# Optimization experiments

Measured on AMD Instinct MI355X. Metric: run time of the kernel, lower is better.

The kernel has to match this reference:

```python
import jax, jax.numpy as jnp
import numpy as np

N = 8192
G = 12972
EPS = 1e-5


def setup_inputs() -> dict:
    key = jax.random.key(0)
    ks = jax.random.split(key, 8)
    # solutions: one-hot letters per position -> (N, 26, 5)
    sol_letters = jax.random.randint(ks[0], (N, 5), 0, 26)
    sols = jax.nn.one_hot(sol_letters, 26, dtype=jnp.float32).transpose(0, 2, 1)
    # guess vocabulary: one-hot words -> (G, 130) with (26,5) layout flattened
    g_letters = jax.random.randint(ks[1], (G, 5), 0, 26)
    guesses_mat = jax.nn.one_hot(g_letters, 26, dtype=jnp.float32).transpose(0, 2, 1).reshape(G, 130)
    s0 = 1.0 / np.sqrt(292.0)
    sh = 1.0 / np.sqrt(1000.0)
    W0 = jax.random.normal(ks[2], (292, 1000), jnp.float32) * s0
    b0 = jnp.zeros((1000,), jnp.float32)
    gammas = jnp.ones((4, 1000), jnp.float32)
    betas = jnp.zeros((4, 1000), jnp.float32)
    Wh = jax.random.normal(ks[3], (3, 1000, 1000), jnp.float32) * sh
    bh = jnp.zeros((3, 1000), jnp.float32)
    Wout = jax.random.normal(ks[4], (1000, 130), jnp.float32) * sh
    bout = jnp.zeros((130,), jnp.float32)
    return {"sols": sols, "guesses_mat": guesses_mat, "W0": W0, "b0": b0,
            "gammas": gammas, "betas": betas, "Wh": Wh, "bh": bh,
            "Wout": Wout, "bout": bout}


def _mlp(X, W0, b0, gammas, betas, Wh, bh, Wout, bout):
    h = X @ W0 + b0
    for i in range(4):
        mu = h.mean(axis=0)
        var = ((h - mu) ** 2).mean(axis=0)  # biased variance, as torch BN training
        h = gammas[i] * (h - mu) * jax.lax.rsqrt(var + EPS) + betas[i]
        h = jnp.where(h >= 0, h, 0.2 * h)
        if i < 3:
            h = h @ Wh[i] + bh[i]
        else:
            h = h @ Wout + bout
    return h


def reference(sols, guesses_mat, W0, b0, gammas, betas, Wh, bh, Wout, bout):
    n = sols.shape[0]
    hints = jnp.zeros((n, 286), jnp.float32)
    scores = 7.0 * jnp.ones((n,), jnp.float32)
    total_loss = jnp.float32(0.0)
    first_guess = None
    solved = jnp.zeros((n,), bool)
    sols_letters = jnp.clip(sols.sum(axis=2), 0.0, 1.0)[:, :, None]  # (n,26,1)
    for turn in range(6):
        turn_vec = jnp.zeros((n, 6), jnp.float32).at[:, turn].set(1.0)
        X = jnp.concatenate((hints, turn_vec), axis=1)  # (n, 292)
        y = _mlp(X, W0, b0, gammas, betas, Wh, bh, Wout, bout).reshape(n, 26, 5)
        logp = jax.nn.log_softmax(y, axis=1)
        loss = -(sols * logp).sum(axis=1).mean()
        if turn >= 1:
            total_loss = total_loss + loss
        y_soft = jax.nn.softmax(y, axis=1).reshape(n, 130)
        # nearest-guess retrieval: argmax over vocab of dot products, then gather
        sim = y_soft @ guesses_mat.T  # (n, G)
        idx = jnp.argmax(sim, axis=1)
        nudges = jax.lax.stop_gradient(guesses_mat[idx] - y_soft)
        guesses = (y_soft + nudges).reshape(n, 26, 5)
        if turn == 0:
            first_guess = guesses[0]
        greens = guesses * sols
        yellows = (1.0 - greens) * (guesses * sols_letters)
        blacks = (guesses * (1.0 - greens) * (1.0 - yellows)).sum(axis=2)  # (n,26)
        solved = greens.reshape(n, -1).sum(axis=1) == 5.0
        new_hints = jnp.concatenate((greens.reshape(n, 130), yellows.reshape(n, 130), blacks), axis=1)
        hints = hints + new_hints
        scores = jnp.where((scores > turn + 1) & solved, jnp.float32(turn + 1), scores)
    return total_loss, scores.sum(), solved.sum(), first_guess
```

## Files before the change

kernel.cpp:

```cpp
#include <hip/hip_runtime.h>

#define NROWS 8192
#define NG    12972
#define H     1000
#define NP    1024
#define KX    288
#define OCP   256
#define OC    130
#define EPSBN 1e-5f
#define MBLK  (NROWS / 128)

typedef __attribute__((ext_vector_type(8))) _Float16 f16x8;
typedef __attribute__((ext_vector_type(8))) unsigned short u16x8;
typedef __attribute__((ext_vector_type(4))) float f32x4;

__device__ __forceinline__ float lrelu(float x) { return x >= 0.f ? x : 0.2f * x; }

__global__ void transpose_f16(const float* __restrict__ src, int R, int C, int srcStride,
                              _Float16* __restrict__ dst, int Rp, int Cp) {
    __shared__ float tile[32][33];
    int k0 = blockIdx.x * 32;
    int n0 = blockIdx.y * 32;
    int tx = threadIdx.x, ty = threadIdx.y;
#pragma unroll
    for (int i = 0; i < 32; i += 8) {
        int k = k0 + ty + i, n = n0 + tx;
        tile[ty + i][tx] = (k < R && n < C) ? src[(size_t)k * srcStride + n] : 0.f;
    }
    __syncthreads();
#pragma unroll
    for (int i = 0; i < 32; i += 8) {
        int n = n0 + ty + i, k = k0 + tx;
        if (n < Cp && k < Rp) dst[(size_t)n * Rp + k] = (_Float16)tile[tx][ty + i];
    }
}

__global__ void prep_bias(const float* __restrict__ W0, const float* __restrict__ b0,
                          const float* __restrict__ bh, const float* __restrict__ bout,
                          float* __restrict__ b0p, float* __restrict__ w0t,
                          float* __restrict__ bhp, float* __restrict__ boutp) {
    int i = blockIdx.x * 256 + threadIdx.x;
    if (i < 1024) { b0p[i] = (i < H) ? b0[i] : 0.f; return; }
    i -= 1024;
    if (i < 6 * 1024) {
        int t = i >> 10, n = i & 1023;
        w0t[i] = (n < H) ? W0[(size_t)(286 + t) * H + n] : 0.f;
        return;
    }
    i -= 6 * 1024;
    if (i < 3 * 1024) {
        int l = i >> 10, n = i & 1023;
        bhp[i] = (n < H) ? bh[l * H + n] : 0.f;
        return;
    }
    i -= 3 * 1024;
    if (i < OCP) { boutp[i] = (i < OC) ? bout[i] : 0.f; }
}

__global__ void prep_guess_letters(const float* __restrict__ gm, unsigned char* __restrict__ gl,
                                   uint2* __restrict__ glp) {
    int g = blockIdx.x * blockDim.x + threadIdx.x;
    if (g >= NG) return;
    unsigned off[5];
    for (int p = 0; p < 5; ++p) {
        int letter = 0;
        for (int c = 0; c < 26; ++c)
            if (gm[(size_t)g * 130 + c * 5 + p] > 0.5f) { letter = c; break; }
        gl[g * 8 + p] = (unsigned char)letter;
        off[p] = (unsigned)(letter * 5 + p);
    }
    gl[g * 8 + 5] = gl[g * 8 + 6] = gl[g * 8 + 7] = 0;
    glp[g] = make_uint2(off[0] | (off[1] << 8) | (off[2] << 16) | (off[3] << 24), off[4]);
}

__global__ void prep_sol_letters(const float* __restrict__ sols, unsigned char* __restrict__ sl,
                                 unsigned int* __restrict__ msk) {
    int r = blockIdx.x * blockDim.x + threadIdx.x;
    if (r >= NROWS) return;
    unsigned int m = 0;
    for (int p = 0; p < 5; ++p) {
        int letter = 0;
        for (int c = 0; c < 26; ++c)
            if (sols[(size_t)r * 130 + c * 5 + p] > 0.5f) { letter = c; break; }
        sl[r * 8 + p] = (unsigned char)letter;
        m |= 1u << letter;
    }
    sl[r * 8 + 5] = sl[r * 8 + 6] = sl[r * 8 + 7] = 0;
    msk[r] = m;
}

__global__ void init_state(unsigned short* __restrict__ hX, float* __restrict__ scores,
                           int* __restrict__ solvedf, float* __restrict__ lossacc) {
    int i = blockIdx.x * blockDim.x + threadIdx.x;
    if (i < NROWS * KX) hX[i] = 0;
    if (i < NROWS) { scores[i] = 7.f; solvedf[i] = 0; }
    if (i == 0) lossacc[0] = 0.f;
}

template <int BK, bool HALF_C>
__global__ __launch_bounds__(256, 2) void gemm_f16(
    const _Float16* __restrict__ A, int lda,
    const _Float16* __restrict__ B, int ldb,
    void* __restrict__ Cv, int ldc,
    const float* __restrict__ bias1, const float* __restrict__ bias2, int kiter,
    float* __restrict__ pS, float* __restrict__ pS2) {
    constexpr int NCH = BK / 8;
    constexpr int ABYTES = 256 * BK;
    constexpr int KSUB = BK / 32;
    constexpr int AW = 16 * BK;
    __shared__ char smem[512 * BK];
    const int tid = threadIdx.x;
    const int lane = tid & 63;
    const int rowBase = blockIdx.x * 128;
    const int colBase = blockIdx.y * 128;
    const int wm = (tid >> 6) & 1;
    const int wn = tid >> 7;

    const _Float16* gsrc[NCH];
    int ldsuni[NCH];
#pragma unroll
    for (int i = 0; i < NCH; ++i) {
        int w = i * 256 + tid;
        const _Float16* plane;
        int off;
        if (w < AW) {
            int r = w & 127, kb = w >> 7;
            plane = A;
            off = (rowBase + r) * lda + kb * 8;
        } else {
            int v = w - AW;
            int col = v & 127, kb = v >> 7;
            plane = B;
            off = (colBase + col) * ldb + kb * 8;
        }
        gsrc[i] = plane + off;
        ldsuni[i] = (i * 256 + (tid & ~63)) * 16;
    }

    f32x4 acc[4][4];
    const f32x4 z = {0.f, 0.f, 0.f, 0.f};
#pragma unroll
    for (int m = 0; m < 4; ++m)
#pragma unroll
        for (int n = 0; n < 4; ++n) acc[m][n] = z;

    const int aro = (lane >> 4) * 2048 + (wm * 64 + (lane & 15)) * 16;
    const int bco = ABYTES + (lane >> 4) * 2048 + (wn * 64 + (lane & 15)) * 16;

    for (int t = 0; t < kiter; ++t) {
#pragma unroll
        for (int i = 0; i < NCH; ++i)
            __builtin_amdgcn_global_load_lds(
                (const __attribute__((address_space(1))) void*)(gsrc[i] + (size_t)t * BK),
                (__attribute__((address_space(3))) void*)(smem + ldsuni[i]), 16, 0, 0);
        __syncthreads();

        f16x8 a_f[KSUB][4], b_f[KSUB][4];
#pragma unroll
        for (int ks = 0; ks < KSUB; ++ks) {
#pragma unroll
            for (int m = 0; m < 4; ++m) a_f[ks][m] = *(const f16x8*)(smem + ks * 8192 + aro + m * 256);
#pragma unroll
            for (int n = 0; n < 4; ++n) b_f[ks][n] = *(const f16x8*)(smem + ks * 8192 + bco + n * 256);
        }
#pragma unroll
        for (int ks = 0; ks < KSUB; ++ks)
#pragma unroll
            for (int m = 0; m < 4; ++m)
#pragma unroll
                for (int n = 0; n < 4; ++n)
                    acc[m][n] = __builtin_amdgcn_mfma_f32_16x16x32_f16(a_f[ks][m], b_f[ks][n],
                                                                       acc[m][n], 0, 0, 0);
        __syncthreads();
    }

    float* sS  = (float*)smem;
    float* sS2 = (float*)smem + 256;
    const int lane16 = lane & 15, lanehi = lane >> 4;
#pragma unroll
    for (int n = 0; n < 4; ++n) {
        int col = colBase + wn * 64 + n * 16 + lane16;
        float bv = bias1[col] + (bias2 ? bias2[col] : 0.f);
        float s = 0.f, s2 = 0.f;
#pragma unroll
        for (int m = 0; m < 4; ++m) {
            int row0 = rowBase + wm * 64 + m * 16 + lanehi * 4;
#pragma unroll
            for (int r = 0; r < 4; ++r) {
                float cv = acc[m][n][r] + bv;
                if constexpr (HALF_C)
                    ((_Float16*)Cv)[(size_t)(row0 + r) * ldc + col] = (_Float16)cv;
                else
                    ((float*)Cv)[(size_t)(row0 + r) * ldc + col] = cv;
                s += cv; s2 += cv * cv;
            }
        }
        if (pS) {
            s += __shfl_xor(s, 16);  s += __shfl_xor(s, 32);
            s2 += __shfl_xor(s2, 16); s2 += __shfl_xor(s2, 32);
            if (lanehi == 0) {
                int lcol = wn * 64 + n * 16 + lane16;
                sS[wm * 128 + lcol] = s;
                sS2[wm * 128 + lcol] = s2;
            }
        }
    }
    if (pS) {
        __syncthreads();
        if (tid < 128) {
            int col = colBase + tid;
            pS[(size_t)blockIdx.x * NP + col] = sS[tid] + sS[128 + tid];
            pS2[(size_t)blockIdx.x * NP + col] = sS2[tid] + sS2[128 + tid];
        }
    }
}

__global__ __launch_bounds__(256) void bn_apply_f(
    const _Float16* __restrict__ hraw, const float* __restrict__ pS, const float* __restrict__ pS2,
    const float* __restrict__ gamma, const float* __restrict__ beta,
    _Float16* __restrict__ oh) {
    __shared__ float la[128], lb[128];
    const int tid = threadIdx.x;
    const int rowBase = blockIdx.x * 128;
    const int colBase = blockIdx.y * 128;
    if (tid < 128) {
        int col = colBase + tid;
        float s = 0.f;
        for (int j = 0; j < MBLK; ++j) s += pS[(size_t)j * NP + col];
        la[tid] = s;
    } else {
        int col = colBase + tid - 128;
        float s2 = 0.f;
        for (int j = 0; j < MBLK; ++j) s2 += pS2[(size_t)j * NP + col];
        lb[tid - 128] = s2;
    }
    __syncthreads();
    if (tid < 128) {
        int col = colBase + tid;
        float a = 0.f, b = 0.f;
        if (col < H) {
            float mean = la[tid] * (1.f / NROWS);
            float var = lb[tid] * (1.f / NROWS) - mean * mean;
            float inv = rsqrtf(var + EPSBN);
            a = gamma[col] * inv;
            b = beta[col] - mean * a;
        }
        la[tid] = a;
        lb[tid] = b;
    }
    __syncthreads();
    const int c8 = (tid & 15) * 8;
    float ar[8], br[8];
#pragma unroll
    for (int j = 0; j < 8; ++j) { ar[j] = la[c8 + j]; br[j] = lb[c8 + j]; }
#pragma unroll
    for (int i = 0; i < 8; ++i) {
        int row = i * 16 + (tid >> 4);
        const u16x8 v = *(const u16x8*)(hraw + (size_t)(rowBase + row) * NP + colBase + c8);
        u16x8 o;
#pragma unroll
        for (int j = 0; j < 8; ++j) {
            float x = (float)__builtin_bit_cast(_Float16, (unsigned short)v[j]);
            o[j] = __builtin_bit_cast(unsigned short, (_Float16)lrelu(ar[j] * x + br[j]));
        }
        *(u16x8*)((unsigned short*)oh + (size_t)(rowBase + row) * NP + colBase + c8) = o;
    }
}

__global__ __launch_bounds__(256) void post_turn(
    const float* __restrict__ ybuf, const uint2* __restrict__ glp,
    const unsigned char* __restrict__ gl, const unsigned char* __restrict__ sl,
    const unsigned int* __restrict__ msk, _Float16* __restrict__ hX,
    float* __restrict__ scores, int* __restrict__ solvedf, float* __restrict__ lossacc,
    const float* __restrict__ gm, float* __restrict__ dout, int turn) {
    const int r0 = blockIdx.x * 8;
    __shared__ float pk[8][132];
    __shared__ float lcon[40];
    __shared__ float wb[4][8];
    __shared__ int wi[4][8];
    __shared__ int fidx[8];
    const int tid = threadIdx.x;

    if (tid < 40) {
        int row = tid / 5, p = tid - row * 5;
        const float* yr = ybuf + (size_t)(r0 + row) * OCP + p;
        float m = -1e30f;
#pragma unroll
        for (int c = 0; c < 26; ++c) m = fmaxf(m, yr[c * 5]);
        float e[26];
        float s = 0.f;
#pragma unroll
        for (int c = 0; c < 26; ++c) { e[c] = expf(yr[c * 5] - m); s += e[c]; }
        float inv = 1.f / s;
#pragma unroll
        for (int c = 0; c < 26; ++c) pk[row][c * 5 + p] = e[c] * inv;
        lcon[tid] = logf(s) + m - yr[sl[(size_t)(r0 + row) * 8 + p] * 5];
    }
    __syncthreads();

    float bb[8];
    int ii[8];
#pragma unroll
    for (int r = 0; r < 8; ++r) { bb[r] = -1e30f; ii[r] = 1 << 30; }
    for (int g = tid; g < NG; g += 256) {
        uint2 w = glp[g];
        int o0 = w.x & 255, o1 = (w.x >> 8) & 255, o2 = (w.x >> 16) & 255,
            o3 = w.x >> 24, o4 = w.y & 255;
#pragma unroll
        for (int r = 0; r < 8; ++r) {
            float v = pk[r][o0] + pk[r][o1]; v += pk[r][o2]; v += pk[r][o3]; v += pk[r][o4];
            if (v > bb[r]) { bb[r] = v; ii[r] = g; }
        }
    }
#pragma unroll
    for (int off = 1; off < 64; off <<= 1) {
#pragma unroll
        for (int r = 0; r < 8; ++r) {
            float o = __shfl_xor(bb[r], off);
            int oi = __shfl_xor(ii[r], off);
            if (o > bb[r] || (o == bb[r] && oi < ii[r])) { bb[r] = o; ii[r] = oi; }
        }
    }
    const int wid = tid >> 6, lane = tid & 63;
    if (lane == 0) {
#pragma unroll
        for (int r = 0; r < 8; ++r) { wb[wid][r] = bb[r]; wi[wid][r] = ii[r]; }
    }
    __syncthreads();

    if (tid < 8) {
        float b = wb[0][tid]; int x = wi[0][tid];
#pragma unroll
        for (int wv = 1; wv < 4; ++wv)
            if (wb[wv][tid] > b || (wb[wv][tid] == b && wi[wv][tid] < x)) { b = wb[wv][tid]; x = wi[wv][tid]; }
        fidx[tid] = x;
        int r = r0 + tid;
        const unsigned char* q = gl + x * 8;
        const unsigned char* so = sl + (size_t)r * 8;
        unsigned int mk = msk[r];
        _Float16* hrow = hX + (size_t)r * KX;
        int allg = 1;
#pragma unroll
        for (int p = 0; p < 5; ++p) {
            int g = q[p];
            int off;
            if (g == so[p]) {
                off = g * 5 + p;
            } else {
                allg = 0;
                off = ((mk >> g) & 1u) ? (130 + g * 5 + p) : (260 + g);
            }
            hrow[off] = (_Float16)((float)hrow[off] + 1.f);
        }
        solvedf[r] = allg;
        if (allg && scores[r] > (float)(turn + 1)) scores[r] = (float)(turn + 1);
    }
    if (tid == 16 && turn >= 1) {
        float t = 0.f;
#pragma unroll
        for (int j = 0; j < 40; ++j) t += lcon[j];
        atomicAdd(lossacc, t * (1.f / (NROWS * 5)));
    }
    __syncthreads();
    if (turn == 0 && blockIdx.x == 0 && tid >= 64 && tid < 64 + OC) {
        dout[3 + tid - 64] = gm[(size_t)fidx[0] * OC + (tid - 64)];
    }
}

__global__ void final_reduce(const float* __restrict__ scores, const int* __restrict__ solvedf,
                             const float* __restrict__ lossacc, float* __restrict__ dout) {
    __shared__ float rs[256];
    __shared__ int ri[256];
    int tid = threadIdx.x;
    float s = 0.f;
    int c = 0;
    for (int r = tid; r < NROWS; r += 256) { s += scores[r]; c += solvedf[r]; }
    rs[tid] = s; ri[tid] = c;
    __syncthreads();
    for (int off = 128; off > 0; off >>= 1) {
        if (tid < off) { rs[tid] += rs[tid + off]; ri[tid] += ri[tid + off]; }
        __syncthreads();
    }
    if (tid == 0) {
        dout[0] = lossacc[0];
        dout[1] = rs[0];
        dout[2] = (float)ri[0];
    }
}

extern "C" void kernel_launch(void* const* d_in, const int* in_sizes, int n_in,
                              void* d_out, int out_size, void* d_ws, size_t ws_size,
                              hipStream_t stream) {
    const float* sols   = (const float*)d_in[0];
    const float* gm     = (const float*)d_in[1];
    const float* W0     = (const float*)d_in[2];
    const float* b0     = (const float*)d_in[3];
    const float* gammas = (const float*)d_in[4];
    const float* betas  = (const float*)d_in[5];
    const float* Wh     = (const float*)d_in[6];
    const float* bh     = (const float*)d_in[7];
    const float* Wout   = (const float*)d_in[8];
    const float* bout   = (const float*)d_in[9];
    float* dout = (float*)d_out;

    char* p = (char*)d_ws;
    auto alloc = [&](size_t bytes) { void* r = (void*)p; p += (bytes + 255) & ~(size_t)255; return r; };
    _Float16* hX   = (_Float16*)alloc((size_t)NROWS * KX * 2);
    _Float16* hA   = (_Float16*)alloc((size_t)NROWS * NP * 2);
    _Float16* hraw = (_Float16*)alloc((size_t)NROWS * NP * 2);
    float* ybuf    = (float*)alloc((size_t)NROWS * OCP * 4);
    _Float16* B0T = (_Float16*)alloc((size_t)NP * KX * 2);
    _Float16* WhT = (_Float16*)alloc((size_t)3 * NP * NP * 2);
    _Float16* BoT = (_Float16*)alloc((size_t)OCP * NP * 2);
    float* b0p   = (float*)alloc(NP * 4);
    float* w0t   = (float*)alloc(6 * NP * 4);
    float* bhp   = (float*)alloc(3 * NP * 4);
    float* boutp = (float*)alloc(OCP * 4);
    float* pS    = (float*)alloc((size_t)MBLK * NP * 4);
    float* pS2   = (float*)alloc((size_t)MBLK * NP * 4);
    float* scores  = (float*)alloc(NROWS * 4);
    float* lossacc = (float*)alloc(256);
    int* solvedf = (int*)alloc(NROWS * 4);
    unsigned char* gl = (unsigned char*)alloc(NG * 8);
    uint2* glp = (uint2*)alloc(NG * 8);
    unsigned char* sl = (unsigned char*)alloc(NROWS * 8);
    unsigned int* msk = (unsigned int*)alloc(NROWS * 4);

    transpose_f16<<<dim3(KX / 32, NP / 32), dim3(32, 8), 0, stream>>>(W0, 286, H, H, B0T, KX, NP);
    for (int l = 0; l < 3; ++l)
        transpose_f16<<<dim3(NP / 32, NP / 32), dim3(32, 8), 0, stream>>>(
            Wh + (size_t)l * H * H, H, H, H, WhT + (size_t)l * NP * NP, NP, NP);
    transpose_f16<<<dim3(NP / 32, OCP / 32), dim3(32, 8), 0, stream>>>(Wout, H, OC, OC, BoT, NP, OCP);
    prep_bias<<<41, 256, 0, stream>>>(W0, b0, bh, bout, b0p, w0t, bhp, boutp);
    prep_guess_letters<<<(NG + 255) / 256, 256, 0, stream>>>(gm, gl, glp);
    prep_sol_letters<<<(NROWS + 255) / 256, 256, 0, stream>>>(sols, sl, msk);
    init_state<<<(NROWS * KX + 255) / 256, 256, 0, stream>>>((unsigned short*)hX, scores, solvedf, lossacc);

    for (int t = 0; t < 6; ++t) {
        gemm_f16<32, true><<<dim3(MBLK, NP / 128), 256, 0, stream>>>(
            hX, KX, B0T, KX, hraw, NP, b0p, w0t + t * NP, KX / 32, pS, pS2);
        for (int l = 0; l < 4; ++l) {
            bn_apply_f<<<dim3(MBLK, NP / 128), 256, 0, stream>>>(
                hraw, pS, pS2, gammas + (size_t)l * H, betas + (size_t)l * H, hA);
            if (l < 3) {
                gemm_f16<64, true><<<dim3(MBLK, NP / 128), 256, 0, stream>>>(
                    hA, NP, WhT + (size_t)l * NP * NP, NP, hraw, NP, bhp + l * NP, nullptr,
                    NP / 64, pS, pS2);
            } else {
                gemm_f16<64, false><<<dim3(MBLK, OCP / 128), 256, 0, stream>>>(
                    hA, NP, BoT, NP, ybuf, OCP, boutp, nullptr, NP / 64, nullptr, nullptr);
            }
        }
        post_turn<<<NROWS / 8, 256, 0, stream>>>(ybuf, glp, gl, sl, msk, hX, scores, solvedf,
                                                 lossacc, gm, dout, t);
    }
    final_reduce<<<1, 256, 0, stream>>>(scores, solvedf, lossacc, dout);
}
```

Measured before the change: 1.553 ms.

## Fuse batch-norm apply into GEMM epilogue via grid-wide atomic barrier

Each hidden-layer GEMM now writes its per-block column sums, waits at a grid-wide atomic counter barrier, then reduces the BN statistics and applies BN plus LeakyReLU directly from its accumulators before writing fp16 output. This drops the separate bn_apply kernel and the fp16 round-trip of raw pre-BN activations, and it ping-pongs between two activation buffers. The grid barrier depends on all 512 blocks (64x8 at 2 per CU) being co-resident. If they are not, the kernel can deadlock, and waiting blocks idle at the barrier.

```diff
diff --git a/kernel.cpp b/kernel.cpp
--- a/kernel.cpp
+++ b/kernel.cpp
@@ -90,20 +90,24 @@
 }
 
 __global__ void init_state(unsigned short* __restrict__ hX, float* __restrict__ scores,
-                           int* __restrict__ solvedf, float* __restrict__ lossacc) {
+                           int* __restrict__ solvedf, float* __restrict__ lossacc,
+                           unsigned int* __restrict__ syncw) {
     int i = blockIdx.x * blockDim.x + threadIdx.x;
     if (i < NROWS * KX) hX[i] = 0;
     if (i < NROWS) { scores[i] = 7.f; solvedf[i] = 0; }
     if (i == 0) lossacc[0] = 0.f;
-}
-
-template <int BK, bool HALF_C>
-__global__ __launch_bounds__(256, 2) void gemm_f16(
+    if (i < 24 * 32) syncw[i] = 0;
+}
+
+template <int BK>
+__global__ __launch_bounds__(256, 2) void gemm_bn(
     const _Float16* __restrict__ A, int lda,
     const _Float16* __restrict__ B, int ldb,
-    void* __restrict__ Cv, int ldc,
+    _Float16* __restrict__ out,
     const float* __restrict__ bias1, const float* __restrict__ bias2, int kiter,
-    float* __restrict__ pS, float* __restrict__ pS2) {
+    float* __restrict__ pS, float* __restrict__ pS2,
+    const float* __restrict__ gamma, const float* __restrict__ beta,
+    unsigned int* __restrict__ cnt) {
     constexpr int NCH = BK / 8;
     constexpr int ABYTES = 256 * BK;
     constexpr int KSUB = BK / 32;
@@ -176,53 +180,48 @@
 
     float* sS  = (float*)smem;
     float* sS2 = (float*)smem + 256;
+    float* la  = (float*)smem + 512;
+    float* lb  = (float*)smem + 640;
     const int lane16 = lane & 15, lanehi = lane >> 4;
+    float bvreg[4];
 #pragma unroll
     for (int n = 0; n < 4; ++n) {
         int col = colBase + wn * 64 + n * 16 + lane16;
         float bv = bias1[col] + (bias2 ? bias2[col] : 0.f);
+        bvreg[n] = bv;
         float s = 0.f, s2 = 0.f;
 #pragma unroll
         for (int m = 0; m < 4; ++m) {
-            int row0 = rowBase + wm * 64 + m * 16 + lanehi * 4;
 #pragma unroll
             for (int r = 0; r < 4; ++r) {
                 float cv = acc[m][n][r] + bv;
-                if constexpr (HALF_C)
-                    ((_Float16*)Cv)[(size_t)(row0 + r) * ldc + col] = (_Float16)cv;
-                else
-                    ((float*)Cv)[(size_t)(row0 + r) * ldc + col] = cv;
                 s += cv; s2 += cv * cv;
             }
         }
-        if (pS) {
-            s += __shfl_xor(s, 16);  s += __shfl_xor(s, 32);
-            s2 += __shfl_xor(s2, 16); s2 += __shfl_xor(s2, 32);
-            if (lanehi == 0) {
-                int lcol = wn * 64 + n * 16 + lane16;
-                sS[wm * 128 + lcol] = s;
-                sS2[wm * 128 + lcol] = s2;
-            }
-        }
-    }
-    if (pS) {
-        __syncthreads();
-        if (tid < 128) {
-            int col = colBase + tid;
-            pS[(size_t)blockIdx.x * NP + col] = sS[tid] + sS[128 + tid];
-            pS2[(size_t)blockIdx.x * NP + col] = sS2[tid] + sS2[128 + tid];
-        }
-    }
-}
-
-__global__ __launch_bounds__(256) void bn_apply_f(
-    const _Float16* __restrict__ hraw, const float* __restrict__ pS, const float* __restrict__ pS2,
-    const float* __restrict__ gamma, const float* __restrict__ beta,
-    _Float16* __restrict__ oh) {
-    __shared__ float la[128], lb[128];
-    const int tid = threadIdx.x;
-    const int rowBase = blockIdx.x * 128;
-    const int colBase = blockIdx.y * 128;
+        s += __shfl_xor(s, 16);  s += __shfl_xor(s, 32);
+        s2 += __shfl_xor(s2, 16); s2 += __shfl_xor(s2, 32);
+        if (lanehi == 0) {
+            int lcol = wn * 64 + n * 16 + lane16;
+            sS[wm * 128 + lcol] = s;
+            sS2[wm * 128 + lcol] = s2;
+        }
+    }
+    __syncthreads();
+    if (tid < 128) {
+        int col = colBase + tid;
+        pS[(size_t)blockIdx.x * NP + col] = sS[tid] + sS[128 + tid];
+        pS2[(size_t)blockIdx.x * NP + col] = sS2[tid] + sS2[128 + tid];
+    }
+    __syncthreads();
+
+    const unsigned NB = gridDim.x * gridDim.y;
+    if (tid == 0) {
+        __hip_atomic_fetch_add(cnt, 1u, __ATOMIC_ACQ_REL, __HIP_MEMORY_SCOPE_AGENT);
+        while (__hip_atomic_load(cnt, __ATOMIC_ACQUIRE, __HIP_MEMORY_SCOPE_AGENT) < NB)
+            __builtin_amdgcn_s_sleep(2);
+    }
+    __syncthreads();
+
     if (tid < 128) {
         int col = colBase + tid;
         float s = 0.f;
@@ -249,21 +248,108 @@
         lb[tid] = b;
     }
     __syncthreads();
-    const int c8 = (tid & 15) * 8;
-    float ar[8], br[8];
-#pragma unroll
-    for (int j = 0; j < 8; ++j) { ar[j] = la[c8 + j]; br[j] = lb[c8 + j]; }
-#pragma unroll
-    for (int i = 0; i < 8; ++i) {
-        int row = i * 16 + (tid >> 4);
-        const u16x8 v = *(const u16x8*)(hraw + (size_t)(rowBase + row) * NP + colBase + c8);
-        u16x8 o;
-#pragma unroll
-        for (int j = 0; j < 8; ++j) {
-            float x = (float)__builtin_bit_cast(_Float16, (unsigned short)v[j]);
-            o[j] = __builtin_bit_cast(unsigned short, (_Float16)lrelu(ar[j] * x + br[j]));
-        }
-        *(u16x8*)((unsigned short*)oh + (size_t)(rowBase + row) * NP + colBase + c8) = o;
+
+#pragma unroll
+    for (int n = 0; n < 4; ++n) {
+        int lcol = wn * 64 + n * 16 + lane16;
+        int col = colBase + lcol;
+        float a = la[lcol], b = lb[lcol];
+#pragma unroll
+        for (int m = 0; m < 4; ++m) {
+            int row0 = rowBase + wm * 64 + m * 16 + lanehi * 4;
+#pragma unroll
+            for (int r = 0; r < 4; ++r) {
+                float cv = acc[m][n][r] + bvreg[n];
+                out[(size_t)(row0 + r) * NP + col] = (_Float16)lrelu(a * cv + b);
+            }
+        }
+    }
+}
+
+__global__ __launch_bounds__(256, 2) void gemm_out(
+    const _Float16* __restrict__ A, int lda,
+    const _Float16* __restrict__ B, int ldb,
+    float* __restrict__ C, int ldc,
+    const float* __restrict__ bias1, int kiter) {
+    constexpr int BK = 64, NCH = 8, ABYTES = 256 * BK, KSUB = 2, AW = 16 * BK;
+    __shared__ char smem[512 * BK];
+    const int tid = threadIdx.x;
+    const int lane = tid & 63;
+    const int rowBase = blockIdx.x * 128;
+    const int colBase = blockIdx.y * 128;
+    const int wm = (tid >> 6) & 1;
+    const int wn = tid >> 7;
+
+    const _Float16* gsrc[NCH];
+    int ldsuni[NCH];
+#pragma unroll
+    for (int i = 0; i < NCH; ++i) {
+        int w = i * 256 + tid;
+        const _Float16* plane;
+        int off;
+        if (w < AW) {
+            int r = w & 127, kb = w >> 7;
+            plane = A;
+            off = (rowBase + r) * lda + kb * 8;
+        } else {
+            int v = w - AW;
+            int col = v & 127, kb = v >> 7;
+            plane = B;
+            off = (colBase + col) * ldb + kb * 8;
+        }
+        gsrc[i] = plane + off;
+        ldsuni[i] = (i * 256 + (tid & ~63)) * 16;
+    }
+
+    f32x4 acc[4][4];
+    const f32x4 z = {0.f, 0.f, 0.f, 0.f};
+#pragma unroll
+    for (int m = 0; m < 4; ++m)
+#pragma unroll
+        for (int n = 0; n < 4; ++n) acc[m][n] = z;
+
+    const int aro = (lane >> 4) * 2048 + (wm * 64 + (lane & 15)) * 16;
+    const int bco = ABYTES + (lane >> 4) * 2048 + (wn * 64 + (lane & 15)) * 16;
+
+    for (int t = 0; t < kiter; ++t) {
+#pragma unroll
+        for (int i = 0; i < NCH; ++i)
+            __builtin_amdgcn_global_load_lds(
+                (const __attribute__((address_space(1))) void*)(gsrc[i] + (size_t)t * BK),
+                (__attribute__((address_space(3))) void*)(smem + ldsuni[i]), 16, 0, 0);
+        __syncthreads();
+
+        f16x8 a_f[KSUB][4], b_f[KSUB][4];
+#pragma unroll
+        for (int ks = 0; ks < KSUB; ++ks) {
+#pragma unroll
+            for (int m = 0; m < 4; ++m) a_f[ks][m] = *(const f16x8*)(smem + ks * 8192 + aro + m * 256);
+#pragma unroll
+            for (int n = 0; n < 4; ++n) b_f[ks][n] = *(const f16x8*)(smem + ks * 8192 + bco + n * 256);
+        }
+#pragma unroll
+        for (int ks = 0; ks < KSUB; ++ks)
+#pragma unroll
+            for (int m = 0; m < 4; ++m)
+#pragma unroll
+                for (int n = 0; n < 4; ++n)
+                    acc[m][n] = __builtin_amdgcn_mfma_f32_16x16x32_f16(a_f[ks][m], b_f[ks][n],
+                                                                       acc[m][n], 0, 0, 0);
+        __syncthreads();
+    }
+
+    const int lane16 = lane & 15, lanehi = lane >> 4;
+#pragma unroll
+    for (int n = 0; n < 4; ++n) {
+        int col = colBase + wn * 64 + n * 16 + lane16;
+        float bv = bias1[col];
+#pragma unroll
+        for (int m = 0; m < 4; ++m) {
+            int row0 = rowBase + wm * 64 + m * 16 + lanehi * 4;
+#pragma unroll
+            for (int r = 0; r < 4; ++r)
+                C[(size_t)(row0 + r) * ldc + col] = acc[m][n][r] + bv;
+        }
     }
 }
 
@@ -405,10 +491,10 @@
 
     char* p = (char*)d_ws;
     auto alloc = [&](size_t bytes) { void* r = (void*)p; p += (bytes + 255) & ~(size_t)255; return r; };
-    _Float16* hX   = (_Float16*)alloc((size_t)NROWS * KX * 2);
-    _Float16* hA   = (_Float16*)alloc((size_t)NROWS * NP * 2);
-    _Float16* hraw = (_Float16*)alloc((size_t)NROWS * NP * 2);
-    float* ybuf    = (float*)alloc((size_t)NROWS * OCP * 4);
+    _Float16* hX  = (_Float16*)alloc((size_t)NROWS * KX * 2);
+    _Float16* hA  = (_Float16*)alloc((size_t)NROWS * NP * 2);
+    _Float16* hB  = (_Float16*)alloc((size_t)NROWS * NP * 2);
+    float* ybuf   = (float*)alloc((size_t)NROWS * OCP * 4);
     _Float16* B0T = (_Float16*)alloc((size_t)NP * KX * 2);
     _Float16* WhT = (_Float16*)alloc((size_t)3 * NP * NP * 2);
     _Float16* BoT = (_Float16*)alloc((size_t)OCP * NP * 2);
@@ -421,6 +507,7 @@
     float* scores  = (float*)alloc(NROWS * 4);
     float* lossacc = (float*)alloc(256);
     int* solvedf = (int*)alloc(NROWS * 4);
+    unsigned int* syncw = (unsigned int*)alloc(24 * 32 * 4);
     unsigned char* gl = (unsigned char*)alloc(NG * 8);
     uint2* glp = (uint2*)alloc(NG * 8);
     unsigned char* sl = (unsigned char*)alloc(NROWS * 8);
@@ -434,23 +521,24 @@
     prep_bias<<<41, 256, 0, stream>>>(W0, b0, bh, bout, b0p, w0t, bhp, boutp);
     prep_guess_letters<<<(NG + 255) / 256, 256, 0, stream>>>(gm, gl, glp);
     prep_sol_letters<<<(NROWS + 255) / 256, 256, 0, stream>>>(sols, sl, msk);
-    init_state<<<(NROWS * KX + 255) / 256, 256, 0, stream>>>((unsigned short*)hX, scores, solvedf, lossacc);
+    init_state<<<(NROWS * KX + 255) / 256, 256, 0, stream>>>((unsigned short*)hX, scores, solvedf,
+                                                             lossacc, syncw);
 
     for (int t = 0; t < 6; ++t) {
-        gemm_f16<32, true><<<dim3(MBLK, NP / 128), 256, 0, stream>>>(
-            hX, KX, B0T, KX, hraw, NP, b0p, w0t + t * NP, KX / 32, pS, pS2);
-        for (int l = 0; l < 4; ++l) {
-            bn_apply_f<<<dim3(MBLK, NP / 128), 256, 0, stream>>>(
-                hraw, pS, pS2, gammas + (size_t)l * H, betas + (size_t)l * H, hA);
-            if (l < 3) {
-                gemm_f16<64, true><<<dim3(MBLK, NP / 128), 256, 0, stream>>>(
-                    hA, NP, WhT + (size_t)l * NP * NP, NP, hraw, NP, bhp + l * NP, nullptr,
-                    NP / 64, pS, pS2);
-            } else {
-                gemm_f16<64, false><<<dim3(MBLK, OCP / 128), 256, 0, stream>>>(
-                    hA, NP, BoT, NP, ybuf, OCP, boutp, nullptr, NP / 64, nullptr, nullptr);
-            }
-        }
+        gemm_bn<32><<<dim3(MBLK, NP / 128), 256, 0, stream>>>(
+            hX, KX, B0T, KX, hA, b0p, w0t + t * NP, KX / 32, pS, pS2,
+            gammas, betas, syncw + (t * 4 + 0) * 32);
+        gemm_bn<64><<<dim3(MBLK, NP / 128), 256, 0, stream>>>(
+            hA, NP, WhT, NP, hB, bhp, nullptr, NP / 64, pS, pS2,
+            gammas + H, betas + H, syncw + (t * 4 + 1) * 32);
+        gemm_bn<64><<<dim3(MBLK, NP / 128), 256, 0, stream>>>(
+            hB, NP, WhT + (size_t)NP * NP, NP, hA, bhp + NP, nullptr, NP / 64, pS, pS2,
+            gammas + 2 * H, betas + 2 * H, syncw + (t * 4 + 2) * 32);
+        gemm_bn<64><<<dim3(MBLK, NP / 128), 256, 0, stream>>>(
+            hA, NP, WhT + (size_t)2 * NP * NP, NP, hB, bhp + 2 * NP, nullptr, NP / 64, pS, pS2,
+            gammas + 3 * H, betas + 3 * H, syncw + (t * 4 + 3) * 32);
+        gemm_out<<<dim3(MBLK, OCP / 128), 256, 0, stream>>>(
+            hB, NP, BoT, NP, ybuf, OCP, boutp, NP / 64);
         post_turn<<<NROWS / 8, 256, 0, stream>>>(ybuf, glp, gl, sl, msk, hX, scores, solvedf,
                                                  lossacc, gm, dout, t);
     }
```

Measured after the change: 2.217 ms. 42.7% more time.

## Compute turn-zero MLP and retrieval once since all rows share identical input

Applied to the files above, without the earlier changes.

At turn zero every row has the same input (zero hints plus the same turn vector), so the MLP and the guess argmax are computed for a single 128-row block. Batch statistics are reconstructed by reading that block's partial sums with stride zero. A single-block kernel finds the shared first guess, and a light per-row kernel applies the hints. This removes roughly one sixth of the GEMM and retrieval work, at the cost of relying on the structural identity of turn-zero rows.

```diff
diff --git a/kernel.cpp b/kernel.cpp
--- a/kernel.cpp
+++ b/kernel.cpp
@@ -218,7 +218,7 @@
 __global__ __launch_bounds__(256) void bn_apply_f(
     const _Float16* __restrict__ hraw, const float* __restrict__ pS, const float* __restrict__ pS2,
     const float* __restrict__ gamma, const float* __restrict__ beta,
-    _Float16* __restrict__ oh) {
+    _Float16* __restrict__ oh, int psjStride) {
     __shared__ float la[128], lb[128];
     const int tid = threadIdx.x;
     const int rowBase = blockIdx.x * 128;
@@ -226,12 +226,12 @@
     if (tid < 128) {
         int col = colBase + tid;
         float s = 0.f;
-        for (int j = 0; j < MBLK; ++j) s += pS[(size_t)j * NP + col];
+        for (int j = 0; j < MBLK; ++j) s += pS[(size_t)j * psjStride + col];
         la[tid] = s;
     } else {
         int col = colBase + tid - 128;
         float s2 = 0.f;
-        for (int j = 0; j < MBLK; ++j) s2 += pS2[(size_t)j * NP + col];
+        for (int j = 0; j < MBLK; ++j) s2 += pS2[(size_t)j * psjStride + col];
         lb[tid - 128] = s2;
     }
     __syncthreads();
@@ -365,6 +365,89 @@
     if (turn == 0 && blockIdx.x == 0 && tid >= 64 && tid < 64 + OC) {
         dout[3 + tid - 64] = gm[(size_t)fidx[0] * OC + (tid - 64)];
     }
+}
+
+__global__ __launch_bounds__(256) void post_turn0(
+    const float* __restrict__ ybuf, const uint2* __restrict__ glp,
+    const float* __restrict__ gm, float* __restrict__ dout, int* __restrict__ idx0buf) {
+    __shared__ float pk[132];
+    __shared__ float wb[4];
+    __shared__ int wi[4];
+    __shared__ int fidx;
+    const int tid = threadIdx.x;
+    if (tid < 5) {
+        int p = tid;
+        const float* yr = ybuf + p;
+        float m = -1e30f;
+#pragma unroll
+        for (int c = 0; c < 26; ++c) m = fmaxf(m, yr[c * 5]);
+        float e[26];
+        float s = 0.f;
+#pragma unroll
+        for (int c = 0; c < 26; ++c) { e[c] = expf(yr[c * 5] - m); s += e[c]; }
+        float inv = 1.f / s;
+#pragma unroll
+        for (int c = 0; c < 26; ++c) pk[c * 5 + p] = e[c] * inv;
+    }
+    __syncthreads();
+    float b = -1e30f;
+    int bi = 1 << 30;
+    for (int g = tid; g < NG; g += 256) {
+        uint2 w = glp[g];
+        int o0 = w.x & 255, o1 = (w.x >> 8) & 255, o2 = (w.x >> 16) & 255,
+            o3 = w.x >> 24, o4 = w.y & 255;
+        float v = pk[o0] + pk[o1]; v += pk[o2]; v += pk[o3]; v += pk[o4];
+        if (v > b) { b = v; bi = g; }
+    }
+#pragma unroll
+    for (int off = 1; off < 64; off <<= 1) {
+        float o = __shfl_xor(b, off);
+        int oi = __shfl_xor(bi, off);
+        if (o > b || (o == b && oi < bi)) { b = o; bi = oi; }
+    }
+    const int wid = tid >> 6, lane = tid & 63;
+    if (lane == 0) { wb[wid] = b; wi[wid] = bi; }
+    __syncthreads();
+    if (tid == 0) {
+        float bx = wb[0]; int x = wi[0];
+#pragma unroll
+        for (int wv = 1; wv < 4; ++wv)
+            if (wb[wv] > bx || (wb[wv] == bx && wi[wv] < x)) { bx = wb[wv]; x = wi[wv]; }
+        fidx = x;
+        idx0buf[0] = x;
+    }
+    __syncthreads();
+    if (tid >= 64 && tid < 64 + OC) {
+        dout[3 + tid - 64] = gm[(size_t)fidx * OC + (tid - 64)];
+    }
+}
+
+__global__ void hints0(const int* __restrict__ idx0buf, const unsigned char* __restrict__ gl,
+                       const unsigned char* __restrict__ sl, const unsigned int* __restrict__ msk,
+                       _Float16* __restrict__ hX, float* __restrict__ scores,
+                       int* __restrict__ solvedf) {
+    int r = blockIdx.x * 256 + threadIdx.x;
+    if (r >= NROWS) return;
+    int x = idx0buf[0];
+    const unsigned char* q = gl + x * 8;
+    const unsigned char* so = sl + (size_t)r * 8;
+    unsigned int mk = msk[r];
+    _Float16* hrow = hX + (size_t)r * KX;
+    int allg = 1;
+#pragma unroll
+    for (int p = 0; p < 5; ++p) {
+        int g = q[p];
+        int off;
+        if (g == so[p]) {
+            off = g * 5 + p;
+        } else {
+            allg = 0;
+            off = ((mk >> g) & 1u) ? (130 + g * 5 + p) : (260 + g);
+        }
+        hrow[off] = (_Float16)((float)hrow[off] + 1.f);
+    }
+    solvedf[r] = allg;
+    if (allg && scores[r] > 1.f) scores[r] = 1.f;
 }
 
 __global__ void final_reduce(const float* __restrict__ scores, const int* __restrict__ solvedf,
@@ -421,6 +504,7 @@
     float* scores  = (float*)alloc(NROWS * 4);
     float* lossacc = (float*)alloc(256);
     int* solvedf = (int*)alloc(NROWS * 4);
+    int* idx0buf = (int*)alloc(256);
     unsigned char* gl = (unsigned char*)alloc(NG * 8);
     uint2* glp = (uint2*)alloc(NG * 8);
     unsigned char* sl = (unsigned char*)alloc(NROWS * 8);
@@ -437,22 +521,29 @@
     init_state<<<(NROWS * KX + 255) / 256, 256, 0, stream>>>((unsigned short*)hX, scores, solvedf, lossacc);
 
     for (int t = 0; t < 6; ++t) {
-        gemm_f16<32, true><<<dim3(MBLK, NP / 128), 256, 0, stream>>>(
+        const int mg = (t == 0) ? 1 : MBLK;
+        const int psStride = (t == 0) ? 0 : NP;
+        gemm_f16<32, true><<<dim3(mg, NP / 128), 256, 0, stream>>>(
             hX, KX, B0T, KX, hraw, NP, b0p, w0t + t * NP, KX / 32, pS, pS2);
         for (int l = 0; l < 4; ++l) {
-            bn_apply_f<<<dim3(MBLK, NP / 128), 256, 0, stream>>>(
-                hraw, pS, pS2, gammas + (size_t)l * H, betas + (size_t)l * H, hA);
+            bn_apply_f<<<dim3(mg, NP / 128), 256, 0, stream>>>(
+                hraw, pS, pS2, gammas + (size_t)l * H, betas + (size_t)l * H, hA, psStride);
             if (l < 3) {
-                gemm_f16<64, true><<<dim3(MBLK, NP / 128), 256, 0, stream>>>(
+                gemm_f16<64, true><<<dim3(mg, NP / 128), 256, 0, stream>>>(
                     hA, NP, WhT + (size_t)l * NP * NP, NP, hraw, NP, bhp + l * NP, nullptr,
                     NP / 64, pS, pS2);
             } else {
-                gemm_f16<64, false><<<dim3(MBLK, OCP / 128), 256, 0, stream>>>(
+                gemm_f16<64, false><<<dim3(mg, OCP / 128), 256, 0, stream>>>(
                     hA, NP, BoT, NP, ybuf, OCP, boutp, nullptr, NP / 64, nullptr, nullptr);
             }
         }
-        post_turn<<<NROWS / 8, 256, 0, stream>>>(ybuf, glp, gl, sl, msk, hX, scores, solvedf,
-                                                 lossacc, gm, dout, t);
+        if (t == 0) {
+            post_turn0<<<1, 256, 0, stream>>>(ybuf, glp, gm, dout, idx0buf);
+            hints0<<<NROWS / 256, 256, 0, stream>>>(idx0buf, gl, sl, msk, hX, scores, solvedf);
+        } else {
+            post_turn<<<NROWS / 8, 256, 0, stream>>>(ybuf, glp, gl, sl, msk, hX, scores, solvedf,
+                                                     lossacc, gm, dout, t);
+        }
     }
     final_reduce<<<1, 256, 0, stream>>>(scores, solvedf, lossacc, dout);
 }
```

Result: faster. 1.487 ms (-4.3%).
